# Performance work log

Hardware: AMD Instinct MI355X
Metric: run time of the kernel (lower is better)

Reference implementation:

```python
import jax, jax.numpy as jnp
import numpy as np

N_NODES = 50000
N_EDGES = 600000
IN_FEATS = 128
HIDDEN = 256
OUT_FEATS = 64


def setup_inputs() -> dict:
    key = jax.random.key(0)
    ks = jax.random.split(key, 12)
    inv = lambda n: 1.0 / np.sqrt(n)
    return {
        "x": jax.random.normal(ks[0], (N_NODES, IN_FEATS), dtype=jnp.float32),
        "edge_index": jax.random.randint(ks[1], (2, N_EDGES), 0, N_NODES, dtype=jnp.int64),
        "W_sage": jax.random.normal(ks[2], (IN_FEATS, IN_FEATS), dtype=jnp.float32) * inv(IN_FEATS),
        "W1a": jax.random.normal(ks[3], (IN_FEATS, HIDDEN), dtype=jnp.float32) * inv(IN_FEATS),
        "b1a": jax.random.normal(ks[4], (HIDDEN,), dtype=jnp.float32) * 0.01,
        "W1b": jax.random.normal(ks[5], (HIDDEN, OUT_FEATS), dtype=jnp.float32) * inv(HIDDEN),
        "b1b": jax.random.normal(ks[6], (OUT_FEATS,), dtype=jnp.float32) * 0.01,
        "W2a": jax.random.normal(ks[7], (IN_FEATS, HIDDEN), dtype=jnp.float32) * inv(IN_FEATS),
        "b2a": jax.random.normal(ks[8], (HIDDEN,), dtype=jnp.float32) * 0.01,
        "W2b": jax.random.normal(ks[9], (HIDDEN, OUT_FEATS), dtype=jnp.float32) * inv(HIDDEN),
        "b2b": jax.random.normal(ks[10], (OUT_FEATS,), dtype=jnp.float32) * 0.01,
    }


def reference(x, edge_index, W_sage, W1a, b1a, W1b, b1b, W2a, b2a, W2b, b2b):
    n = x.shape[0]
    src, dst = edge_index[0], edge_index[1]
    # SAGEConv mean aggregation: mean over incoming neighbor (source) features at each target node
    summed = jax.ops.segment_sum(x[src], dst, num_segments=n)          # [N, in]
    deg = jax.ops.segment_sum(jnp.ones_like(src, dtype=x.dtype), dst, num_segments=n)
    mean = summed / jnp.maximum(deg, 1.0)[:, None]                     # nodes w/o neighbors -> 0
    x_1hop = mean @ W_sage                                             # lin_l, no root, no bias
    # dual MLP branches (dropout is identity in eval mode)
    out1 = jax.nn.relu(x @ W1a + b1a) @ W1b + b1b
    out2 = jax.nn.relu(x_1hop @ W2a + b2a) @ W2b + b2b
    return out1 + out2
```

## Files before the change

kernel.cpp:

```cpp
#include <hip/hip_runtime.h>

#define N_NODES 50000
#define N_EDGES 600000
#define IN_F 128
#define HID 256
#define OUT_F 64
#define ROWS 16
#define SLOTS 56

typedef __attribute__((ext_vector_type(8))) short bf16x8;
typedef __attribute__((ext_vector_type(4))) float f32x4;

__device__ inline short f2bf(float f) {
    unsigned u = __builtin_bit_cast(unsigned, f);
    u += 0x7fffu + ((u >> 16) & 1u);
    return (short)(u >> 16);
}
__device__ inline float bflo(unsigned u) { return __builtin_bit_cast(float, u << 16); }
__device__ inline float bfhi(unsigned u) { return __builtin_bit_cast(float, u & 0xffff0000u); }

__global__ __launch_bounds__(256) void prep_kernel(
    const float* __restrict__ x, short* __restrict__ xb,
    const float* __restrict__ Wsg, const float* __restrict__ W1a,
    const float* __restrict__ W1b, const float* __restrict__ W2a,
    const float* __restrict__ W2b,
    short* __restrict__ Fsg, short* __restrict__ F1a, short* __restrict__ F1b,
    short* __restrict__ F2a, short* __restrict__ F2b,
    int* __restrict__ cursor)
{
    const int bid = blockIdx.x, t = threadIdx.x;
    if (bid < 3125) {
        int i = bid * 256 + t;
        float4 a0 = *reinterpret_cast<const float4*>(x + (size_t)i * 8);
        float4 a1 = *reinterpret_cast<const float4*>(x + (size_t)i * 8 + 4);
        bf16x8 v;
        v[0] = f2bf(a0.x); v[1] = f2bf(a0.y); v[2] = f2bf(a0.z); v[3] = f2bf(a0.w);
        v[4] = f2bf(a1.x); v[5] = f2bf(a1.y); v[6] = f2bf(a1.z); v[7] = f2bf(a1.w);
        *reinterpret_cast<bf16x8*>(xb + (size_t)i * 8) = v;
    } else if (bid < 3181) {
        int cid = (bid - 3125) * 256 + t;
        const float* src; short* dst; int N, KST, base;
        if      (cid < 2048)  { src = Wsg; dst = Fsg; N = 128; KST = 4; base = 0; }
        else if (cid < 6144)  { src = W1a; dst = F1a; N = 256; KST = 4; base = 2048; }
        else if (cid < 8192)  { src = W1b; dst = F1b; N = 64;  KST = 8; base = 6144; }
        else if (cid < 12288) { src = W2a; dst = F2a; N = 256; KST = 4; base = 8192; }
        else                  { src = W2b; dst = F2b; N = 64;  KST = 8; base = 12288; }
        int c = cid - base;
        int lane = c & 63;
        int rem = c >> 6;
        int ks = rem % KST;
        int nt = rem / KST;
        int col = nt * 16 + (lane & 15);
        int k0 = ks * 32 + (lane >> 4) * 8;
        bf16x8 v;
        #pragma unroll
        for (int j = 0; j < 8; ++j)
            v[j] = f2bf(src[(size_t)(k0 + j) * N + col]);
        *reinterpret_cast<bf16x8*>(dst + (size_t)c * 8) = v;
    } else {
        for (int i = (bid - 3181) * 256 + t; i < N_NODES; i += 19 * 256)
            cursor[i] = 0;
    }
}

__global__ __launch_bounds__(256) void build_kernel(
    const int* __restrict__ ei, int* __restrict__ cursor, int* __restrict__ esrc)
{
    int e = blockIdx.x * 256 + threadIdx.x;
    if (e >= N_EDGES) return;
    int src = ei[e];
    int dst = ei[N_EDGES + e];
    int p = atomicAdd(&cursor[dst], 1);
    if (p < SLOTS) esrc[(size_t)dst * SLOTS + p] = src;
}

__device__ inline bf16x8 afrag_lds128(const short* S, int lane, int ks) {
    int row = lane & 15, g = lane >> 4;
    int chunk = (ks * 4 + g) ^ row;
    return *reinterpret_cast<const bf16x8*>(
        reinterpret_cast<const char*>(S) + row * 256 + chunk * 16);
}
__device__ inline bf16x8 afrag_lds256(const short* S, int lane, int ks) {
    int row = lane & 15, g = lane >> 4;
    int chunk = (ks * 4 + g) ^ row;
    return *reinterpret_cast<const bf16x8*>(
        reinterpret_cast<const char*>(S) + row * 512 + chunk * 16);
}

__device__ inline void stage1_relu(const bf16x8 afr[4], short* Hs,
                                   const short* __restrict__ Waf,
                                   const float* __restrict__ ba,
                                   int w, int lane)
{
    const int row16 = lane & 15, g = lane >> 4;
    #pragma unroll
    for (int i = 0; i < 4; ++i) {
        int nt = w * 4 + i;
        f32x4 acc = {0.f, 0.f, 0.f, 0.f};
        #pragma unroll
        for (int ks = 0; ks < 4; ++ks) {
            bf16x8 b = *reinterpret_cast<const bf16x8*>(
                Waf + ((size_t)(nt * 4 + ks) * 64 + lane) * 8);
            acc = __builtin_amdgcn_mfma_f32_16x16x32_bf16(afr[ks], b, acc, 0, 0, 0);
        }
        int col = nt * 16 + row16;
        float bias = ba[col];
        #pragma unroll
        for (int reg = 0; reg < 4; ++reg) {
            int hrow = g * 4 + reg;
            float v = fmaxf(acc[reg] + bias, 0.0f);
            *reinterpret_cast<short*>(reinterpret_cast<char*>(Hs)
                + hrow * 512 + (((col >> 3) ^ hrow) & 31) * 16 + (col & 7) * 2) = f2bf(v);
        }
    }
}

__device__ inline f32x4 stage2_acc(const short* Hs, const short* __restrict__ Wbf,
                                   int w, int lane, f32x4 acc)
{
    #pragma unroll
    for (int ks = 0; ks < 8; ++ks) {
        bf16x8 a = afrag_lds256(Hs, lane, ks);
        bf16x8 b = *reinterpret_cast<const bf16x8*>(
            Wbf + ((size_t)(w * 8 + ks) * 64 + lane) * 8);
        acc = __builtin_amdgcn_mfma_f32_16x16x32_bf16(a, b, acc, 0, 0, 0);
    }
    return acc;
}

__global__ __launch_bounds__(256) void fused_kernel(
    const short* __restrict__ xb, const int* __restrict__ esrc,
    const int* __restrict__ deg,
    const short* __restrict__ Fsg,
    const short* __restrict__ F1a, const float* __restrict__ b1a,
    const short* __restrict__ F1b, const float* __restrict__ b1b,
    const short* __restrict__ F2a, const float* __restrict__ b2a,
    const short* __restrict__ F2b, const float* __restrict__ b2b,
    float* __restrict__ out)
{
    __shared__ short Ms[16 * 128];
    __shared__ short Xs[16 * 128];
    __shared__ short Hs[16 * 256];
    const int t = threadIdx.x, w = t >> 6, lane = t & 63;
    const long r0 = (long)blockIdx.x * ROWS;
    const int row16 = lane & 15, g = lane >> 4;

    #pragma unroll
    for (int nn = 0; nn < 4; ++nn) {
        int row = w * 4 + nn;
        long node = r0 + row;
        int d = deg[node]; if (d > SLOTS) d = SLOTS;
        int my = (lane < SLOTS) ? esrc[(size_t)node * SLOTS + lane] : 0;
        float ax = 0.f, ay = 0.f;
        for (int j = 0; j < d; j += 16) {
            unsigned u[16];
            #pragma unroll
            for (int k = 0; k < 16; ++k) {
                int idx = j + k;
                int cidx = idx < d ? idx : d - 1;
                int s = __builtin_amdgcn_readlane(my, cidx);
                u[k] = *reinterpret_cast<const unsigned*>(xb + (size_t)s * IN_F + lane * 2);
            }
            #pragma unroll
            for (int k = 0; k < 16; ++k) {
                float wk = (j + k < d) ? 1.0f : 0.0f;
                ax = fmaf(bflo(u[k]), wk, ax);
                ay = fmaf(bfhi(u[k]), wk, ay);
            }
        }
        float inv = (d > 0) ? 1.0f / (float)d : 0.0f;
        ax *= inv; ay *= inv;
        int chunk = (lane >> 2) ^ row;
        unsigned packed = (unsigned)(unsigned short)f2bf(ax)
                        | ((unsigned)(unsigned short)f2bf(ay) << 16);
        *reinterpret_cast<unsigned*>(reinterpret_cast<char*>(Ms)
            + row * 256 + chunk * 16 + (lane & 3) * 4) = packed;
    }
    __syncthreads();

    #pragma unroll
    for (int i = 0; i < 2; ++i) {
        int nt = w * 2 + i;
        f32x4 acc = {0.f, 0.f, 0.f, 0.f};
        #pragma unroll
        for (int ks = 0; ks < 4; ++ks) {
            bf16x8 a = afrag_lds128(Ms, lane, ks);
            bf16x8 b = *reinterpret_cast<const bf16x8*>(
                Fsg + ((size_t)(nt * 4 + ks) * 64 + lane) * 8);
            acc = __builtin_amdgcn_mfma_f32_16x16x32_bf16(a, b, acc, 0, 0, 0);
        }
        int col = nt * 16 + row16;
        #pragma unroll
        for (int reg = 0; reg < 4; ++reg) {
            int xrow = g * 4 + reg;
            *reinterpret_cast<short*>(reinterpret_cast<char*>(Xs)
                + xrow * 256 + (((col >> 3) ^ xrow) & 15) * 16 + (col & 7) * 2)
                = f2bf(acc[reg]);
        }
    }
    __syncthreads();

    {
        bf16x8 afr[4];
        const short* xrow = xb + (size_t)(r0 + row16) * IN_F + g * 8;
        #pragma unroll
        for (int ks = 0; ks < 4; ++ks)
            afr[ks] = *reinterpret_cast<const bf16x8*>(xrow + ks * 32);
        stage1_relu(afr, Hs, F1a, b1a, w, lane);
    }
    __syncthreads();

    f32x4 oacc = {0.f, 0.f, 0.f, 0.f};
    oacc = stage2_acc(Hs, F1b, w, lane, oacc);
    __syncthreads();

    {
        bf16x8 afr[4];
        #pragma unroll
        for (int ks = 0; ks < 4; ++ks) afr[ks] = afrag_lds128(Xs, lane, ks);
        stage1_relu(afr, Hs, F2a, b2a, w, lane);
    }
    __syncthreads();

    oacc = stage2_acc(Hs, F2b, w, lane, oacc);
    {
        int col = w * 16 + row16;
        float bias = b1b[col] + b2b[col];
        #pragma unroll
        for (int reg = 0; reg < 4; ++reg)
            out[(size_t)(r0 + g * 4 + reg) * OUT_F + col] = oacc[reg] + bias;
    }
}

extern "C" void kernel_launch(void* const* d_in, const int* in_sizes, int n_in,
                              void* d_out, int out_size, void* d_ws, size_t ws_size,
                              hipStream_t stream)
{
    const float* x   = (const float*)d_in[0];
    const int*   ei  = (const int*)d_in[1];
    const float* Wsg = (const float*)d_in[2];
    const float* W1a = (const float*)d_in[3];
    const float* b1a = (const float*)d_in[4];
    const float* W1b = (const float*)d_in[5];
    const float* b1b = (const float*)d_in[6];
    const float* W2a = (const float*)d_in[7];
    const float* b2a = (const float*)d_in[8];
    const float* W2b = (const float*)d_in[9];
    const float* b2b = (const float*)d_in[10];
    float* out = (float*)d_out;

    int* cursor = (int*)d_ws;
    int* esrc   = cursor + 50048;
    short* Fsg  = (short*)(esrc + (size_t)N_NODES * SLOTS);
    short* F1a  = Fsg + 2048 * 8;
    short* F1b  = F1a + 4096 * 8;
    short* F2a  = F1b + 2048 * 8;
    short* F2b  = F2a + 4096 * 8;
    short* xb   = F2b + 2048 * 8;

    prep_kernel<<<3200, 256, 0, stream>>>(x, xb, Wsg, W1a, W1b, W2a, W2b,
                                          Fsg, F1a, F1b, F2a, F2b, cursor);
    build_kernel<<<(N_EDGES + 255) / 256, 256, 0, stream>>>(ei, cursor, esrc);
    fused_kernel<<<N_NODES / ROWS, 256, 0, stream>>>(xb, esrc, cursor, Fsg,
                                                     F1a, b1a, F1b, b1b,
                                                     F2a, b2a, F2b, b2b, out);
}
```

Baseline: 101.9 us.

## Merge prep and build kernels and double the rows per fused block

The graph-building atomics move into the prep kernel, and the cursor zeroing becomes a memset. This saves one kernel launch and the serial dependency between prep and build. The fused kernel now handles 32 rows per block as two MFMA M-tiles, so each weight fragment loaded from global memory is reused twice. The neighbour gather now processes two nodes per wave, one per half-wave, with 8-byte loads. The cost is more registers and LDS per block, fewer blocks, and padded tail rows that read past the real node count.

```diff
diff --git a/kernel.cpp b/kernel.cpp
--- a/kernel.cpp
+++ b/kernel.cpp
@@ -1,12 +1,14 @@
 #include <hip/hip_runtime.h>
 
 #define N_NODES 50000
+#define N_PAD   50048
 #define N_EDGES 600000
 #define IN_F 128
 #define HID 256
 #define OUT_F 64
-#define ROWS 16
+#define ROWS 32
 #define SLOTS 56
+#define NBLK ((N_NODES + ROWS - 1) / ROWS)
 
 typedef __attribute__((ext_vector_type(8))) short bf16x8;
 typedef __attribute__((ext_vector_type(4))) float f32x4;
@@ -19,14 +21,14 @@
 __device__ inline float bflo(unsigned u) { return __builtin_bit_cast(float, u << 16); }
 __device__ inline float bfhi(unsigned u) { return __builtin_bit_cast(float, u & 0xffff0000u); }
 
-__global__ __launch_bounds__(256) void prep_kernel(
+__global__ __launch_bounds__(256) void prep_build_kernel(
     const float* __restrict__ x, short* __restrict__ xb,
     const float* __restrict__ Wsg, const float* __restrict__ W1a,
     const float* __restrict__ W1b, const float* __restrict__ W2a,
     const float* __restrict__ W2b,
     short* __restrict__ Fsg, short* __restrict__ F1a, short* __restrict__ F1b,
     short* __restrict__ F2a, short* __restrict__ F2b,
-    int* __restrict__ cursor)
+    const int* __restrict__ ei, int* __restrict__ cursor, int* __restrict__ esrc)
 {
     const int bid = blockIdx.x, t = threadIdx.x;
     if (bid < 3125) {
@@ -58,74 +60,66 @@
             v[j] = f2bf(src[(size_t)(k0 + j) * N + col]);
         *reinterpret_cast<bf16x8*>(dst + (size_t)c * 8) = v;
     } else {
-        for (int i = (bid - 3181) * 256 + t; i < N_NODES; i += 19 * 256)
-            cursor[i] = 0;
-    }
-}
-
-__global__ __launch_bounds__(256) void build_kernel(
-    const int* __restrict__ ei, int* __restrict__ cursor, int* __restrict__ esrc)
-{
-    int e = blockIdx.x * 256 + threadIdx.x;
-    if (e >= N_EDGES) return;
-    int src = ei[e];
-    int dst = ei[N_EDGES + e];
-    int p = atomicAdd(&cursor[dst], 1);
-    if (p < SLOTS) esrc[(size_t)dst * SLOTS + p] = src;
-}
-
-__device__ inline bf16x8 afrag_lds128(const short* S, int lane, int ks) {
-    int row = lane & 15, g = lane >> 4;
-    int chunk = (ks * 4 + g) ^ row;
-    return *reinterpret_cast<const bf16x8*>(
-        reinterpret_cast<const char*>(S) + row * 256 + chunk * 16);
-}
-__device__ inline bf16x8 afrag_lds256(const short* S, int lane, int ks) {
-    int row = lane & 15, g = lane >> 4;
-    int chunk = (ks * 4 + g) ^ row;
-    return *reinterpret_cast<const bf16x8*>(
-        reinterpret_cast<const char*>(S) + row * 512 + chunk * 16);
-}
-
-__device__ inline void stage1_relu(const bf16x8 afr[4], short* Hs,
-                                   const short* __restrict__ Waf,
-                                   const float* __restrict__ ba,
-                                   int w, int lane)
+        int e = (bid - 3181) * 256 + t;
+        if (e < N_EDGES) {
+            int src = ei[e];
+            int dst = ei[N_EDGES + e];
+            int p = atomicAdd(&cursor[dst], 1);
+            if (p < SLOTS) esrc[(size_t)dst * SLOTS + p] = src;
+        }
+    }
+}
+
+__device__ inline void stage1_relu2(const bf16x8 afr[2][4], short* Hs,
+                                    const short* __restrict__ Waf,
+                                    const float* __restrict__ ba,
+                                    int w, int lane)
 {
     const int row16 = lane & 15, g = lane >> 4;
     #pragma unroll
     for (int i = 0; i < 4; ++i) {
         int nt = w * 4 + i;
-        f32x4 acc = {0.f, 0.f, 0.f, 0.f};
-        #pragma unroll
-        for (int ks = 0; ks < 4; ++ks) {
-            bf16x8 b = *reinterpret_cast<const bf16x8*>(
+        bf16x8 bfr[4];
+        #pragma unroll
+        for (int ks = 0; ks < 4; ++ks)
+            bfr[ks] = *reinterpret_cast<const bf16x8*>(
                 Waf + ((size_t)(nt * 4 + ks) * 64 + lane) * 8);
-            acc = __builtin_amdgcn_mfma_f32_16x16x32_bf16(afr[ks], b, acc, 0, 0, 0);
-        }
         int col = nt * 16 + row16;
         float bias = ba[col];
         #pragma unroll
-        for (int reg = 0; reg < 4; ++reg) {
-            int hrow = g * 4 + reg;
-            float v = fmaxf(acc[reg] + bias, 0.0f);
-            *reinterpret_cast<short*>(reinterpret_cast<char*>(Hs)
-                + hrow * 512 + (((col >> 3) ^ hrow) & 31) * 16 + (col & 7) * 2) = f2bf(v);
-        }
-    }
-}
-
-__device__ inline f32x4 stage2_acc(const short* Hs, const short* __restrict__ Wbf,
-                                   int w, int lane, f32x4 acc)
-{
+        for (int mt = 0; mt < 2; ++mt) {
+            f32x4 acc = {0.f, 0.f, 0.f, 0.f};
+            #pragma unroll
+            for (int ks = 0; ks < 4; ++ks)
+                acc = __builtin_amdgcn_mfma_f32_16x16x32_bf16(afr[mt][ks], bfr[ks], acc, 0, 0, 0);
+            #pragma unroll
+            for (int reg = 0; reg < 4; ++reg) {
+                int hrow = mt * 16 + g * 4 + reg;
+                float v = fmaxf(acc[reg] + bias, 0.0f);
+                *reinterpret_cast<short*>(reinterpret_cast<char*>(Hs)
+                    + hrow * 512 + ((((col >> 3) ^ hrow) & 31) * 16) + (col & 7) * 2) = f2bf(v);
+            }
+        }
+    }
+}
+
+__device__ inline void stage2_acc2(const short* Hs, const short* __restrict__ Wbf,
+                                   int w, int lane, f32x4 oacc[2])
+{
+    const int g = lane >> 4, row16 = lane & 15;
     #pragma unroll
     for (int ks = 0; ks < 8; ++ks) {
-        bf16x8 a = afrag_lds256(Hs, lane, ks);
         bf16x8 b = *reinterpret_cast<const bf16x8*>(
             Wbf + ((size_t)(w * 8 + ks) * 64 + lane) * 8);
-        acc = __builtin_amdgcn_mfma_f32_16x16x32_bf16(a, b, acc, 0, 0, 0);
-    }
-    return acc;
+        #pragma unroll
+        for (int mt = 0; mt < 2; ++mt) {
+            int arow = mt * 16 + row16;
+            bf16x8 a = *reinterpret_cast<const bf16x8*>(
+                reinterpret_cast<const char*>(Hs)
+                + arow * 512 + ((((ks * 4 + g) ^ arow) & 31) * 16));
+            oacc[mt] = __builtin_amdgcn_mfma_f32_16x16x32_bf16(a, b, oacc[mt], 0, 0, 0);
+        }
+    }
 }
 
 __global__ __launch_bounds__(256) void fused_kernel(
@@ -138,97 +132,136 @@
     const short* __restrict__ F2b, const float* __restrict__ b2b,
     float* __restrict__ out)
 {
-    __shared__ short Ms[16 * 128];
-    __shared__ short Xs[16 * 128];
-    __shared__ short Hs[16 * 256];
+    __shared__ short Ms[ROWS * 128];
+    __shared__ short Xs[ROWS * 128];
+    __shared__ short Hs[ROWS * 256];
     const int t = threadIdx.x, w = t >> 6, lane = t & 63;
+    const int l31 = lane & 31, half = lane >> 5;
+    const int row16 = lane & 15, g = lane >> 4;
     const long r0 = (long)blockIdx.x * ROWS;
-    const int row16 = lane & 15, g = lane >> 4;
 
     #pragma unroll
-    for (int nn = 0; nn < 4; ++nn) {
-        int row = w * 4 + nn;
-        long node = r0 + row;
-        int d = deg[node]; if (d > SLOTS) d = SLOTS;
-        int my = (lane < SLOTS) ? esrc[(size_t)node * SLOTS + lane] : 0;
-        float ax = 0.f, ay = 0.f;
-        for (int j = 0; j < d; j += 16) {
-            unsigned u[16];
+    for (int p = 0; p < 4; ++p) {
+        int rowA = w * 8 + p * 2;
+        int myrow = rowA + half;
+        long nodeA = r0 + rowA;
+        int dv = deg[r0 + myrow]; dv = min(dv, SLOTS);
+        int dA = __builtin_amdgcn_readlane(dv, 0);
+        int dB = __builtin_amdgcn_readlane(dv, 32);
+        int slot = lane < SLOTS ? lane : SLOTS - 1;
+        int myA = esrc[(size_t)nodeA * SLOTS + slot];
+        int myB = esrc[(size_t)(nodeA + 1) * SLOTS + slot];
+        int dAm = max(dA - 1, 0), dBm = max(dB - 1, 0);
+        int dmax = max(dA, dB);
+        float a0 = 0.f, a1 = 0.f, a2 = 0.f, a3 = 0.f;
+        for (int j = 0; j < dmax; j += 16) {
+            uint2 u[16];
             #pragma unroll
             for (int k = 0; k < 16; ++k) {
-                int idx = j + k;
-                int cidx = idx < d ? idx : d - 1;
-                int s = __builtin_amdgcn_readlane(my, cidx);
-                u[k] = *reinterpret_cast<const unsigned*>(xb + (size_t)s * IN_F + lane * 2);
+                int kA = min(j + k, dAm), kB = min(j + k, dBm);
+                int sA = __builtin_amdgcn_readlane(myA, kA);
+                int sB = __builtin_amdgcn_readlane(myB, kB);
+                sA = (dA > 0) ? sA : 0;
+                sB = (dB > 0) ? sB : 0;
+                int s = half ? sB : sA;
+                u[k] = *reinterpret_cast<const uint2*>(xb + (size_t)s * IN_F + l31 * 4);
             }
             #pragma unroll
             for (int k = 0; k < 16; ++k) {
-                float wk = (j + k < d) ? 1.0f : 0.0f;
-                ax = fmaf(bflo(u[k]), wk, ax);
-                ay = fmaf(bfhi(u[k]), wk, ay);
-            }
-        }
-        float inv = (d > 0) ? 1.0f / (float)d : 0.0f;
-        ax *= inv; ay *= inv;
-        int chunk = (lane >> 2) ^ row;
-        unsigned packed = (unsigned)(unsigned short)f2bf(ax)
-                        | ((unsigned)(unsigned short)f2bf(ay) << 16);
-        *reinterpret_cast<unsigned*>(reinterpret_cast<char*>(Ms)
-            + row * 256 + chunk * 16 + (lane & 3) * 4) = packed;
+                float wk = (j + k < dv) ? 1.0f : 0.0f;
+                a0 = fmaf(bflo(u[k].x), wk, a0);
+                a1 = fmaf(bfhi(u[k].x), wk, a1);
+                a2 = fmaf(bflo(u[k].y), wk, a2);
+                a3 = fmaf(bfhi(u[k].y), wk, a3);
+            }
+        }
+        float inv = dv > 0 ? 1.0f / (float)dv : 0.0f;
+        unsigned lo = (unsigned)(unsigned short)f2bf(a0 * inv)
+                    | ((unsigned)(unsigned short)f2bf(a1 * inv) << 16);
+        unsigned hi = (unsigned)(unsigned short)f2bf(a2 * inv)
+                    | ((unsigned)(unsigned short)f2bf(a3 * inv) << 16);
+        int chunk = ((l31 >> 1) ^ (myrow & 15)) & 15;
+        uint2 pk; pk.x = lo; pk.y = hi;
+        *reinterpret_cast<uint2*>(reinterpret_cast<char*>(Ms)
+            + myrow * 256 + chunk * 16 + (l31 & 1) * 8) = pk;
     }
     __syncthreads();
 
     #pragma unroll
     for (int i = 0; i < 2; ++i) {
         int nt = w * 2 + i;
-        f32x4 acc = {0.f, 0.f, 0.f, 0.f};
-        #pragma unroll
-        for (int ks = 0; ks < 4; ++ks) {
-            bf16x8 a = afrag_lds128(Ms, lane, ks);
-            bf16x8 b = *reinterpret_cast<const bf16x8*>(
+        bf16x8 bfr[4];
+        #pragma unroll
+        for (int ks = 0; ks < 4; ++ks)
+            bfr[ks] = *reinterpret_cast<const bf16x8*>(
                 Fsg + ((size_t)(nt * 4 + ks) * 64 + lane) * 8);
-            acc = __builtin_amdgcn_mfma_f32_16x16x32_bf16(a, b, acc, 0, 0, 0);
-        }
-        int col = nt * 16 + row16;
-        #pragma unroll
-        for (int reg = 0; reg < 4; ++reg) {
-            int xrow = g * 4 + reg;
-            *reinterpret_cast<short*>(reinterpret_cast<char*>(Xs)
-                + xrow * 256 + (((col >> 3) ^ xrow) & 15) * 16 + (col & 7) * 2)
-                = f2bf(acc[reg]);
+        #pragma unroll
+        for (int mt = 0; mt < 2; ++mt) {
+            f32x4 acc = {0.f, 0.f, 0.f, 0.f};
+            #pragma unroll
+            for (int ks = 0; ks < 4; ++ks) {
+                int arow = mt * 16 + row16;
+                bf16x8 a = *reinterpret_cast<const bf16x8*>(
+                    reinterpret_cast<const char*>(Ms)
+                    + arow * 256 + ((((ks * 4 + g) ^ arow) & 15) * 16));
+                acc = __builtin_amdgcn_mfma_f32_16x16x32_bf16(a, bfr[ks], acc, 0, 0, 0);
+            }
+            int col = nt * 16 + row16;
+            #pragma unroll
+            for (int reg = 0; reg < 4; ++reg) {
+                int xrow = mt * 16 + g * 4 + reg;
+                *reinterpret_cast<short*>(reinterpret_cast<char*>(Xs)
+                    + xrow * 256 + ((((col >> 3) ^ xrow) & 15) * 16) + (col & 7) * 2)
+                    = f2bf(acc[reg]);
+            }
         }
     }
     __syncthreads();
 
     {
-        bf16x8 afr[4];
-        const short* xrow = xb + (size_t)(r0 + row16) * IN_F + g * 8;
-        #pragma unroll
-        for (int ks = 0; ks < 4; ++ks)
-            afr[ks] = *reinterpret_cast<const bf16x8*>(xrow + ks * 32);
-        stage1_relu(afr, Hs, F1a, b1a, w, lane);
-    }
-    __syncthreads();
-
-    f32x4 oacc = {0.f, 0.f, 0.f, 0.f};
-    oacc = stage2_acc(Hs, F1b, w, lane, oacc);
+        bf16x8 afr[2][4];
+        #pragma unroll
+        for (int mt = 0; mt < 2; ++mt) {
+            const short* xrow = xb + (size_t)(r0 + mt * 16 + row16) * IN_F + g * 8;
+            #pragma unroll
+            for (int ks = 0; ks < 4; ++ks)
+                afr[mt][ks] = *reinterpret_cast<const bf16x8*>(xrow + ks * 32);
+        }
+        stage1_relu2(afr, Hs, F1a, b1a, w, lane);
+    }
+    __syncthreads();
+
+    f32x4 oacc[2] = {{0.f, 0.f, 0.f, 0.f}, {0.f, 0.f, 0.f, 0.f}};
+    stage2_acc2(Hs, F1b, w, lane, oacc);
     __syncthreads();
 
     {
-        bf16x8 afr[4];
-        #pragma unroll
-        for (int ks = 0; ks < 4; ++ks) afr[ks] = afrag_lds128(Xs, lane, ks);
-        stage1_relu(afr, Hs, F2a, b2a, w, lane);
-    }
-    __syncthreads();
-
-    oacc = stage2_acc(Hs, F2b, w, lane, oacc);
+        bf16x8 afr[2][4];
+        #pragma unroll
+        for (int mt = 0; mt < 2; ++mt) {
+            int arow = mt * 16 + row16;
+            #pragma unroll
+            for (int ks = 0; ks < 4; ++ks)
+                afr[mt][ks] = *reinterpret_cast<const bf16x8*>(
+                    reinterpret_cast<const char*>(Xs)
+                    + arow * 256 + ((((ks * 4 + g) ^ arow) & 15) * 16));
+        }
+        stage1_relu2(afr, Hs, F2a, b2a, w, lane);
+    }
+    __syncthreads();
+
+    stage2_acc2(Hs, F2b, w, lane, oacc);
     {
         int col = w * 16 + row16;
         float bias = b1b[col] + b2b[col];
         #pragma unroll
-        for (int reg = 0; reg < 4; ++reg)
-            out[(size_t)(r0 + g * 4 + reg) * OUT_F + col] = oacc[reg] + bias;
+        for (int mt = 0; mt < 2; ++mt)
+            #pragma unroll
+            for (int reg = 0; reg < 4; ++reg) {
+                long row = r0 + mt * 16 + g * 4 + reg;
+                if (row < N_NODES)
+                    out[row * OUT_F + col] = oacc[mt][reg] + bias;
+            }
     }
 }
 
@@ -250,18 +283,19 @@
     float* out = (float*)d_out;
 
     int* cursor = (int*)d_ws;
-    int* esrc   = cursor + 50048;
-    short* Fsg  = (short*)(esrc + (size_t)N_NODES * SLOTS);
+    int* esrc   = cursor + N_PAD;
+    short* Fsg  = (short*)(esrc + (size_t)N_PAD * SLOTS);
     short* F1a  = Fsg + 2048 * 8;
     short* F1b  = F1a + 4096 * 8;
     short* F2a  = F1b + 2048 * 8;
     short* F2b  = F2a + 4096 * 8;
     short* xb   = F2b + 2048 * 8;
 
-    prep_kernel<<<3200, 256, 0, stream>>>(x, xb, Wsg, W1a, W1b, W2a, W2b,
-                                          Fsg, F1a, F1b, F2a, F2b, cursor);
-    build_kernel<<<(N_EDGES + 255) / 256, 256, 0, stream>>>(ei, cursor, esrc);
-    fused_kernel<<<N_NODES / ROWS, 256, 0, stream>>>(xb, esrc, cursor, Fsg,
-                                                     F1a, b1a, F1b, b1b,
-                                                     F2a, b2a, F2b, b2b, out);
-}
+    hipMemsetAsync(cursor, 0, N_PAD * sizeof(int), stream);
+    prep_build_kernel<<<5525, 256, 0, stream>>>(x, xb, Wsg, W1a, W1b, W2a, W2b,
+                                                Fsg, F1a, F1b, F2a, F2b,
+                                                ei, cursor, esrc);
+    fused_kernel<<<NBLK, 256, 0, stream>>>(xb, esrc, cursor, Fsg,
+                                           F1a, b1a, F1b, b1b,
+                                           F2a, b2a, F2b, b2b, out);
+}
```

New measurement: 122.1 us. 19.8% more time.

## Fold SAGE weight into W2a, merge prep and edge build, use 16-bit neighbor indices

Applied to the files above, without the earlier changes.

Adds a small kernel that precomputes Wsg·W2a in fp32, so the fused kernel goes straight from the mean aggregate into the branch-2 hidden layer. This drops the separate x_1hop GEMM stage, its shared buffer and two barriers. The bf16 weight packing, x conversion and edge-bucket build now run in one launch, and neighbor indices are stored as unsigned short to halve index traffic. The grid is padded to a multiple of 16 rows with guarded output stores. In exchange it rounds the folded weight once instead of rounding the intermediate x_1hop, and the padded rows read xb past the real node count.

```diff
diff --git a/kernel.cpp b/kernel.cpp
--- a/kernel.cpp
+++ b/kernel.cpp
@@ -1,12 +1,14 @@
 #include <hip/hip_runtime.h>
 
 #define N_NODES 50000
+#define N_PAD   50048
 #define N_EDGES 600000
 #define IN_F 128
 #define HID 256
 #define OUT_F 64
 #define ROWS 16
 #define SLOTS 56
+#define NBLK (N_PAD / ROWS)
 
 typedef __attribute__((ext_vector_type(8))) short bf16x8;
 typedef __attribute__((ext_vector_type(4))) float f32x4;
@@ -19,14 +21,31 @@
 __device__ inline float bflo(unsigned u) { return __builtin_bit_cast(float, u << 16); }
 __device__ inline float bfhi(unsigned u) { return __builtin_bit_cast(float, u & 0xffff0000u); }
 
-__global__ __launch_bounds__(256) void prep_kernel(
+__global__ __launch_bounds__(256) void k0_kernel(
+    const float* __restrict__ Wsg, const float* __restrict__ W2a,
+    float* __restrict__ Wc, int* __restrict__ cursor)
+{
+    const int bid = blockIdx.x, t = threadIdx.x;
+    if (bid < 128) {
+        float acc = 0.f;
+        #pragma unroll 8
+        for (int j = 0; j < 128; ++j)
+            acc = fmaf(Wsg[bid * 128 + j], W2a[j * 256 + t], acc);
+        Wc[bid * 256 + t] = acc;
+    } else {
+        int i = (bid - 128) * 256 + t;
+        if (i < N_PAD) cursor[i] = 0;
+    }
+}
+
+__global__ __launch_bounds__(256) void prep_build_kernel(
     const float* __restrict__ x, short* __restrict__ xb,
-    const float* __restrict__ Wsg, const float* __restrict__ W1a,
-    const float* __restrict__ W1b, const float* __restrict__ W2a,
-    const float* __restrict__ W2b,
-    short* __restrict__ Fsg, short* __restrict__ F1a, short* __restrict__ F1b,
-    short* __restrict__ F2a, short* __restrict__ F2b,
-    int* __restrict__ cursor)
+    const float* __restrict__ W1a, const float* __restrict__ W1b,
+    const float* __restrict__ Wc,  const float* __restrict__ W2b,
+    short* __restrict__ F1a, short* __restrict__ F1b,
+    short* __restrict__ Fc,  short* __restrict__ F2b,
+    const int* __restrict__ ei, int* __restrict__ cursor,
+    unsigned short* __restrict__ esrc)
 {
     const int bid = blockIdx.x, t = threadIdx.x;
     if (bid < 3125) {
@@ -37,14 +56,13 @@
         v[0] = f2bf(a0.x); v[1] = f2bf(a0.y); v[2] = f2bf(a0.z); v[3] = f2bf(a0.w);
         v[4] = f2bf(a1.x); v[5] = f2bf(a1.y); v[6] = f2bf(a1.z); v[7] = f2bf(a1.w);
         *reinterpret_cast<bf16x8*>(xb + (size_t)i * 8) = v;
-    } else if (bid < 3181) {
+    } else if (bid < 3173) {
         int cid = (bid - 3125) * 256 + t;
         const float* src; short* dst; int N, KST, base;
-        if      (cid < 2048)  { src = Wsg; dst = Fsg; N = 128; KST = 4; base = 0; }
-        else if (cid < 6144)  { src = W1a; dst = F1a; N = 256; KST = 4; base = 2048; }
-        else if (cid < 8192)  { src = W1b; dst = F1b; N = 64;  KST = 8; base = 6144; }
-        else if (cid < 12288) { src = W2a; dst = F2a; N = 256; KST = 4; base = 8192; }
-        else                  { src = W2b; dst = F2b; N = 64;  KST = 8; base = 12288; }
+        if      (cid < 4096)  { src = W1a; dst = F1a; N = 256; KST = 4; base = 0; }
+        else if (cid < 6144)  { src = W1b; dst = F1b; N = 64;  KST = 8; base = 4096; }
+        else if (cid < 10240) { src = Wc;  dst = Fc;  N = 256; KST = 4; base = 6144; }
+        else                  { src = W2b; dst = F2b; N = 64;  KST = 8; base = 10240; }
         int c = cid - base;
         int lane = c & 63;
         int rem = c >> 6;
@@ -58,20 +76,14 @@
             v[j] = f2bf(src[(size_t)(k0 + j) * N + col]);
         *reinterpret_cast<bf16x8*>(dst + (size_t)c * 8) = v;
     } else {
-        for (int i = (bid - 3181) * 256 + t; i < N_NODES; i += 19 * 256)
-            cursor[i] = 0;
-    }
-}
-
-__global__ __launch_bounds__(256) void build_kernel(
-    const int* __restrict__ ei, int* __restrict__ cursor, int* __restrict__ esrc)
-{
-    int e = blockIdx.x * 256 + threadIdx.x;
-    if (e >= N_EDGES) return;
-    int src = ei[e];
-    int dst = ei[N_EDGES + e];
-    int p = atomicAdd(&cursor[dst], 1);
-    if (p < SLOTS) esrc[(size_t)dst * SLOTS + p] = src;
+        int e = (bid - 3173) * 256 + t;
+        if (e < N_EDGES) {
+            int src = ei[e];
+            int dst = ei[N_EDGES + e];
+            int p = atomicAdd(&cursor[dst], 1);
+            if (p < SLOTS) esrc[(size_t)dst * SLOTS + p] = (unsigned short)src;
+        }
+    }
 }
 
 __device__ inline bf16x8 afrag_lds128(const short* S, int lane, int ks) {
@@ -110,7 +122,7 @@
             int hrow = g * 4 + reg;
             float v = fmaxf(acc[reg] + bias, 0.0f);
             *reinterpret_cast<short*>(reinterpret_cast<char*>(Hs)
-                + hrow * 512 + (((col >> 3) ^ hrow) & 31) * 16 + (col & 7) * 2) = f2bf(v);
+                + hrow * 512 + ((((col >> 3) ^ hrow) & 31) * 16) + (col & 7) * 2) = f2bf(v);
         }
     }
 }
@@ -129,17 +141,15 @@
 }
 
 __global__ __launch_bounds__(256) void fused_kernel(
-    const short* __restrict__ xb, const int* __restrict__ esrc,
+    const short* __restrict__ xb, const unsigned short* __restrict__ esrc,
     const int* __restrict__ deg,
-    const short* __restrict__ Fsg,
     const short* __restrict__ F1a, const float* __restrict__ b1a,
     const short* __restrict__ F1b, const float* __restrict__ b1b,
-    const short* __restrict__ F2a, const float* __restrict__ b2a,
+    const short* __restrict__ Fc,  const float* __restrict__ b2a,
     const short* __restrict__ F2b, const float* __restrict__ b2b,
     float* __restrict__ out)
 {
     __shared__ short Ms[16 * 128];
-    __shared__ short Xs[16 * 128];
     __shared__ short Hs[16 * 256];
     const int t = threadIdx.x, w = t >> 6, lane = t & 63;
     const long r0 = (long)blockIdx.x * ROWS;
@@ -149,15 +159,15 @@
     for (int nn = 0; nn < 4; ++nn) {
         int row = w * 4 + nn;
         long node = r0 + row;
-        int d = deg[node]; if (d > SLOTS) d = SLOTS;
-        int my = (lane < SLOTS) ? esrc[(size_t)node * SLOTS + lane] : 0;
+        int d = deg[node]; d = min(d, SLOTS);
+        int slot = min(lane, SLOTS - 1);
+        int my = esrc[(size_t)node * SLOTS + slot];
         float ax = 0.f, ay = 0.f;
         for (int j = 0; j < d; j += 16) {
             unsigned u[16];
             #pragma unroll
             for (int k = 0; k < 16; ++k) {
-                int idx = j + k;
-                int cidx = idx < d ? idx : d - 1;
+                int cidx = min(j + k, d - 1);
                 int s = __builtin_amdgcn_readlane(my, cidx);
                 u[k] = *reinterpret_cast<const unsigned*>(xb + (size_t)s * IN_F + lane * 2);
             }
@@ -178,26 +188,16 @@
     }
     __syncthreads();
 
-    #pragma unroll
-    for (int i = 0; i < 2; ++i) {
-        int nt = w * 2 + i;
-        f32x4 acc = {0.f, 0.f, 0.f, 0.f};
-        #pragma unroll
-        for (int ks = 0; ks < 4; ++ks) {
-            bf16x8 a = afrag_lds128(Ms, lane, ks);
-            bf16x8 b = *reinterpret_cast<const bf16x8*>(
-                Fsg + ((size_t)(nt * 4 + ks) * 64 + lane) * 8);
-            acc = __builtin_amdgcn_mfma_f32_16x16x32_bf16(a, b, acc, 0, 0, 0);
-        }
-        int col = nt * 16 + row16;
-        #pragma unroll
-        for (int reg = 0; reg < 4; ++reg) {
-            int xrow = g * 4 + reg;
-            *reinterpret_cast<short*>(reinterpret_cast<char*>(Xs)
-                + xrow * 256 + (((col >> 3) ^ xrow) & 15) * 16 + (col & 7) * 2)
-                = f2bf(acc[reg]);
-        }
-    }
+    {
+        bf16x8 afr[4];
+        #pragma unroll
+        for (int ks = 0; ks < 4; ++ks) afr[ks] = afrag_lds128(Ms, lane, ks);
+        stage1_relu(afr, Hs, Fc, b2a, w, lane);
+    }
+    __syncthreads();
+
+    f32x4 oacc = {0.f, 0.f, 0.f, 0.f};
+    oacc = stage2_acc(Hs, F2b, w, lane, oacc);
     __syncthreads();
 
     {
@@ -210,25 +210,16 @@
     }
     __syncthreads();
 
-    f32x4 oacc = {0.f, 0.f, 0.f, 0.f};
     oacc = stage2_acc(Hs, F1b, w, lane, oacc);
-    __syncthreads();
-
-    {
-        bf16x8 afr[4];
-        #pragma unroll
-        for (int ks = 0; ks < 4; ++ks) afr[ks] = afrag_lds128(Xs, lane, ks);
-        stage1_relu(afr, Hs, F2a, b2a, w, lane);
-    }
-    __syncthreads();
-
-    oacc = stage2_acc(Hs, F2b, w, lane, oacc);
     {
         int col = w * 16 + row16;
         float bias = b1b[col] + b2b[col];
         #pragma unroll
-        for (int reg = 0; reg < 4; ++reg)
-            out[(size_t)(r0 + g * 4 + reg) * OUT_F + col] = oacc[reg] + bias;
+        for (int reg = 0; reg < 4; ++reg) {
+            long row = r0 + g * 4 + reg;
+            if (row < N_NODES)
+                out[row * OUT_F + col] = oacc[reg] + bias;
+        }
     }
 }
 
@@ -250,18 +241,19 @@
     float* out = (float*)d_out;
 
     int* cursor = (int*)d_ws;
-    int* esrc   = cursor + 50048;
-    short* Fsg  = (short*)(esrc + (size_t)N_NODES * SLOTS);
-    short* F1a  = Fsg + 2048 * 8;
-    short* F1b  = F1a + 4096 * 8;
-    short* F2a  = F1b + 2048 * 8;
-    short* F2b  = F2a + 4096 * 8;
-    short* xb   = F2b + 2048 * 8;
-
-    prep_kernel<<<3200, 256, 0, stream>>>(x, xb, Wsg, W1a, W1b, W2a, W2b,
-                                          Fsg, F1a, F1b, F2a, F2b, cursor);
-    build_kernel<<<(N_EDGES + 255) / 256, 256, 0, stream>>>(ei, cursor, esrc);
-    fused_kernel<<<N_NODES / ROWS, 256, 0, stream>>>(xb, esrc, cursor, Fsg,
-                                                     F1a, b1a, F1b, b1b,
-                                                     F2a, b2a, F2b, b2b, out);
-}
+    unsigned short* esrc = (unsigned short*)(cursor + N_PAD);
+    float* Wc  = (float*)(esrc + (size_t)N_PAD * SLOTS);
+    short* F1a = (short*)(Wc + 128 * 256);
+    short* F1b = F1a + 4096 * 8;
+    short* Fc  = F1b + 2048 * 8;
+    short* F2b = Fc + 4096 * 8;
+    short* xb  = F2b + 2048 * 8;
+
+    k0_kernel<<<324, 256, 0, stream>>>(Wsg, W2a, Wc, cursor);
+    prep_build_kernel<<<5517, 256, 0, stream>>>(x, xb, W1a, W1b, Wc, W2b,
+                                                F1a, F1b, Fc, F2b,
+                                                ei, cursor, esrc);
+    fused_kernel<<<NBLK, 256, 0, stream>>>(xb, esrc, cursor,
+                                           F1a, b1a, F1b, b1b,
+                                           Fc, b2a, F2b, b2b, out);
+}
```

Measured after the change: 119.6 us. 17.4% more time.
